# Optimization experiments

Hardware: AMD Instinct MI355X
Metric: run time of the kernel (lower is better)

Reference implementation:

```python
import jax, jax.numpy as jnp
import numpy as np

N = 50000
E = 800000
IN_CH = 128
HID = 64
HEADS = 4
OUT_CH = 64
NEG_SLOPE = 0.2


def add_self_loops(edge_index, num_nodes):
    loops = jnp.arange(num_nodes, dtype=edge_index.dtype)
    src = jnp.concatenate([edge_index[0], loops])
    dst = jnp.concatenate([edge_index[1], loops])
    return src, dst


def gat_layer(x, src, dst, W, a_src, a_dst, b, heads, out_ch, concat):
    n = x.shape[0]
    h = (x @ W).reshape(n, heads, out_ch)              # [N,H,C]
    al_src = jnp.einsum('nhc,hc->nh', h, a_src)        # [N,H]
    al_dst = jnp.einsum('nhc,hc->nh', h, a_dst)        # [N,H]
    e = jax.nn.leaky_relu(al_src[src] + al_dst[dst], NEG_SLOPE)  # [Et,H]
    # segment softmax over incoming edges of each destination node
    m = jax.ops.segment_max(e, dst, num_segments=n)
    ex = jnp.exp(e - m[dst])
    denom = jax.ops.segment_sum(ex, dst, num_segments=n)
    alpha = ex / (denom[dst] + 1e-16)                  # [Et,H]
    msg = h[src] * alpha[:, :, None]                   # [Et,H,C]
    out = jax.ops.segment_sum(msg, dst, num_segments=n)  # [N,H,C]
    if concat:
        out = out.reshape(n, heads * out_ch)
    else:
        out = out.mean(axis=1)
    return out + b


def setup_inputs() -> dict:
    key = jax.random.key(0)
    ks = jax.random.split(key, 10)
    x = jax.random.normal(ks[0], (N, IN_CH), dtype=jnp.float32)
    edge_index = jax.random.randint(ks[1], (2, E), 0, N, dtype=jnp.int64)
    s1 = 1.0 / np.sqrt(IN_CH)
    W1 = jax.random.normal(ks[2], (IN_CH, HEADS * HID), dtype=jnp.float32) * s1
    a_src1 = jax.random.normal(ks[3], (HEADS, HID), dtype=jnp.float32) * 0.1
    a_dst1 = jax.random.normal(ks[4], (HEADS, HID), dtype=jnp.float32) * 0.1
    b1 = jnp.zeros((HEADS * HID,), dtype=jnp.float32)
    s2 = 1.0 / np.sqrt(HEADS * HID)
    W2 = jax.random.normal(ks[5], (HEADS * HID, OUT_CH), dtype=jnp.float32) * s2
    a_src2 = jax.random.normal(ks[6], (1, OUT_CH), dtype=jnp.float32) * 0.1
    a_dst2 = jax.random.normal(ks[7], (1, OUT_CH), dtype=jnp.float32) * 0.1
    b2 = jnp.zeros((OUT_CH,), dtype=jnp.float32)
    return {"x": x, "edge_index": edge_index, "W1": W1, "a_src1": a_src1,
            "a_dst1": a_dst1, "b1": b1, "W2": W2, "a_src2": a_src2,
            "a_dst2": a_dst2, "b2": b2}


def reference(x, edge_index, W1, a_src1, a_dst1, b1, W2, a_src2, a_dst2, b2):
    src, dst = add_self_loops(edge_index, x.shape[0])
    h = gat_layer(x, src, dst, W1, a_src1, a_dst1, b1, HEADS, HID, True)
    h = jax.nn.elu(h)
    h = gat_layer(h, src, dst, W2, a_src2, a_dst2, b2, 1, OUT_CH, False)
    return jax.nn.elu(h)
```

## Files before the change

kernel.cpp:

```cpp
#include <hip/hip_runtime.h>
#include <hip/hip_bf16.h>
#include <cstdint>
#include <cstddef>


#define CAP 96

typedef float f32x4 __attribute__((ext_vector_type(4)));
typedef __fp16 f16x8 __attribute__((ext_vector_type(8)));

static __device__ __forceinline__ float lrelu02(float x) { return x > 0.f ? x : 0.2f * x; }
static __device__ __forceinline__ float eluf(float x)    { return x > 0.f ? x : __expf(x) - 1.f; }

__global__ __launch_bounds__(256) void kD_kernel(const float* __restrict__ A,
                                                 const float* __restrict__ W1,
                                                 __fp16* __restrict__ C,
                                                 const float* __restrict__ a_src,
                                                 const float* __restrict__ a_dst,
                                                 float* __restrict__ als,
                                                 float* __restrict__ ald,
                                                 const int* __restrict__ ei,
                                                 int* __restrict__ cnt,
                                                 int* __restrict__ sidx,
                                                 const float* __restrict__ W2,
                                                 __fp16* __restrict__ w2t,
                                                 int M, int e, int gb, int cb) {
    __shared__ __fp16 sm[17920];
    int b = blockIdx.x;
    int t = threadIdx.x;
    if (b >= gb) {
        if (b < gb + cb) {
            int* sflag = (int*)sm;
            if (t < 64) {
                int m = e < 64 ? e : 64;
                int z = (t < m && ei[2 * t + 1] == 0) ? 1 : 0;
                unsigned long long bal = __ballot(z);
                if (t == 0) *sflag = (__popcll(bal) >= m / 2 + 1) ? 1 : 0;
            }
            __syncthreads();
            int f = *sflag;
            int i = (b - gb) * 256 + t;
            if (i < e) {
                int s = f ? ei[2 * i] : ei[i];
                int d = f ? ei[2 * (e + i)] : ei[e + i];
                int pos = atomicAdd(&cnt[d], 1);
                if (pos < CAP) sidx[d * CAP + pos] = s;
            }
        } else {
            int j = (b - gb - cb) * 256 + t;
            if (j < 16384) {
                int nn = j >> 8, k = j & 255;
                w2t[j] = (__fp16)W2[k * 64 + nn];
            }
        }
        return;
    }
    #define AS(r, c)  sm[(r) * 40 + (c)]
    #define BST(r, c) sm[2560 + (r) * 40 + (c)]
    #define CS(r, c)  sm[(r) * 264 + (c)]
    float* sa = (float*)(sm + 16896);
    float* sd = (float*)(sm + 17408);
    int wv = t >> 6, l = t & 63;
    int lm = l & 15, kq = l >> 4;
    int bm = b * 64;
    sa[t] = a_src[t];
    sd[t] = a_dst[t];
    f32x4 zero = {0.f, 0.f, 0.f, 0.f};
    f32x4 acc[4][4] = {{zero, zero, zero, zero}, {zero, zero, zero, zero},
                       {zero, zero, zero, zero}, {zero, zero, zero, zero}};
    int arow = t >> 2, achunk = (t & 3) * 8;
    for (int k0 = 0; k0 < 128; k0 += 32) {
        {
            int gr = bm + arow;
            f16x8 av;
            if (gr < M) {
                const float* ap = A + (size_t)gr * 128 + k0 + achunk;
                float4 a0 = *(const float4*)(ap + 0);
                float4 a1 = *(const float4*)(ap + 4);
                av[0] = (__fp16)a0.x; av[1] = (__fp16)a0.y; av[2] = (__fp16)a0.z; av[3] = (__fp16)a0.w;
                av[4] = (__fp16)a1.x; av[5] = (__fp16)a1.y; av[6] = (__fp16)a1.z; av[7] = (__fp16)a1.w;
            } else { f16x8 z = {0,0,0,0,0,0,0,0}; av = z; }
            *(f16x8*)&AS(arow, achunk) = av;
        }
        {
            #pragma unroll
            for (int bc = 0; bc < 4; ++bc) {
                f16x8 bh;
                #pragma unroll
                for (int j = 0; j < 8; ++j)
                    bh[j] = (__fp16)W1[(size_t)(k0 + bc * 8 + j) * 256 + t];
                *(f16x8*)&BST(t, bc * 8) = bh;
            }
        }
        __syncthreads();
        #pragma unroll
        for (int nt = 0; nt < 4; ++nt) {
            f16x8 bfrag = *(const f16x8*)&BST(wv * 64 + nt * 16 + lm, kq * 8);
            #pragma unroll
            for (int mt = 0; mt < 4; ++mt) {
                f16x8 afrag = *(const f16x8*)&AS(mt * 16 + lm, kq * 8);
                acc[mt][nt] = __builtin_amdgcn_mfma_f32_16x16x32_f16(afrag, bfrag, acc[mt][nt], 0, 0, 0);
            }
        }
        __syncthreads();
    }
    #pragma unroll
    for (int mt = 0; mt < 4; ++mt)
        #pragma unroll
        for (int nt = 0; nt < 4; ++nt)
            #pragma unroll
            for (int r = 0; r < 4; ++r)
                CS(mt * 16 + kq * 4 + r, wv * 64 + nt * 16 + lm) = (__fp16)acc[mt][nt][r];
    __syncthreads();
    {
        int row = t >> 2, head = t & 3;
        int gr = bm + row;
        f16x8 c[8];
        #pragma unroll
        for (int q = 0; q < 8; ++q) c[q] = *(const f16x8*)&CS(row, head * 64 + q * 8);
        float ps = 0.f, pd = 0.f;
        #pragma unroll
        for (int q = 0; q < 8; ++q)
            #pragma unroll
            for (int j = 0; j < 8; ++j) {
                float v = (float)c[q][j];
                ps += v * sa[head * 64 + q * 8 + j];
                pd += v * sd[head * 64 + q * 8 + j];
            }
        if (gr < M) {
            f16x8* gp = (f16x8*)(C + (size_t)gr * 256 + head * 64);
            #pragma unroll
            for (int q = 0; q < 8; ++q) gp[q] = c[q];
            als[gr * 4 + head] = ps;
            ald[gr * 4 + head] = pd;
        }
    }
    #undef AS
    #undef BST
    #undef CS
}

__global__ __launch_bounds__(256) void agg1_kernel(const __fp16* __restrict__ h1,
                                                   const int* __restrict__ sidx,
                                                   const int* __restrict__ cnt,
                                                   const float* __restrict__ als,
                                                   const float* __restrict__ ald,
                                                   const float* __restrict__ b1,
                                                   __fp16* __restrict__ x2, int n) {
    int t = threadIdx.x, wv = t >> 6, l = t & 63;
    int node = blockIdx.x * 4 + wv;
    if (node >= n) return;
    int le = l & 31, halfE = l >> 5;
    int head = le >> 3;
    float aldn = ald[node * 4 + head];
    int cn = cnt[node];
    cn = cn < CAP ? cn : CAP;
    int p0 = node * CAP;
    float acc[8] = {0.f, 0.f, 0.f, 0.f, 0.f, 0.f, 0.f, 0.f};
    float accw = 0.f;
    auto bodyS = [&](int s) {
        float wt = __expf(lrelu02(als[s * 4 + head] + aldn));
        accw += wt;
        f16x8 r = *(const f16x8*)(h1 + (size_t)s * 256 + le * 8);
        #pragma unroll
        for (int j = 0; j < 8; ++j) acc[j] += wt * (float)r[j];
    };
    auto body = [&](int p) { bodyS(sidx[p]); };
    int p = p0 + halfE, pend = p0 + cn;
    for (; p + 6 < pend; p += 8) { body(p); body(p + 2); body(p + 4); body(p + 6); }
    for (; p < pend; p += 2) body(p);
    if (halfE == 0) bodyS(node);
    #pragma unroll
    for (int j = 0; j < 8; ++j) acc[j] += __shfl_down(acc[j], 32);
    accw += __shfl_down(accw, 32);
    if (l < 32) {
        float rd = 1.f / (accw + 1e-16f);
        f16x8 o;
        #pragma unroll
        for (int j = 0; j < 8; ++j) {
            float v = acc[j] * rd + b1[le * 8 + j];
            o[j] = (__fp16)eluf(v);
        }
        *(f16x8*)(x2 + (size_t)node * 256 + le * 8) = o;
    }
}

__global__ __launch_bounds__(256) void gemm2_kernel(const __fp16* __restrict__ A,
                                                    const __fp16* __restrict__ w2t,
                                                    __fp16* __restrict__ C,
                                                    const float* __restrict__ a_src,
                                                    const float* __restrict__ a_dst,
                                                    float* __restrict__ als,
                                                    float* __restrict__ ald, int M) {
    __shared__ __fp16 sm[9216];
    #define AS(r, c)  sm[(r) * 72 + (c)]
    #define BST(r, c) sm[4608 + (r) * 72 + (c)]
    #define CS(r, c)  sm[(r) * 72 + (c)]
    int t = threadIdx.x;
    int wv = t >> 6, l = t & 63;
    int lm = l & 15, kq = l >> 4;
    int bm = blockIdx.x * 64;
    f32x4 zero = {0.f, 0.f, 0.f, 0.f};
    f32x4 acc[4] = {zero, zero, zero, zero};
    int arow = t >> 2, akp = (t & 3) * 16;
    int bn = t & 63, bkc = (t >> 6) * 16;
    for (int k0 = 0; k0 < 256; k0 += 64) {
        {
            int gr = bm + arow;
            f16x8 av0, av1;
            if (gr < M) {
                const __fp16* ap = A + (size_t)gr * 256 + k0 + akp;
                av0 = *(const f16x8*)(ap);
                av1 = *(const f16x8*)(ap + 8);
            } else { f16x8 z = {0,0,0,0,0,0,0,0}; av0 = z; av1 = z; }
            *(f16x8*)&AS(arow, akp) = av0;
            *(f16x8*)&AS(arow, akp + 8) = av1;
        }
        {
            const __fp16* bp = w2t + (size_t)bn * 256 + k0 + bkc;
            *(f16x8*)&BST(bn, bkc) = *(const f16x8*)(bp);
            *(f16x8*)&BST(bn, bkc + 8) = *(const f16x8*)(bp + 8);
        }
        __syncthreads();
        #pragma unroll
        for (int ki = 0; ki < 2; ++ki) {
            int kc = ki * 32 + kq * 8;
            f16x8 bfrag = *(const f16x8*)&BST(wv * 16 + lm, kc);
            #pragma unroll
            for (int mt = 0; mt < 4; ++mt) {
                f16x8 afrag = *(const f16x8*)&AS(mt * 16 + lm, kc);
                acc[mt] = __builtin_amdgcn_mfma_f32_16x16x32_f16(afrag, bfrag, acc[mt], 0, 0, 0);
            }
        }
        __syncthreads();
    }
    #pragma unroll
    for (int mt = 0; mt < 4; ++mt)
        #pragma unroll
        for (int r = 0; r < 4; ++r)
            CS(mt * 16 + kq * 4 + r, wv * 16 + lm) = (__fp16)acc[mt][r];
    __syncthreads();
    {
        int row = t >> 2, ch = (t & 3) * 16;
        int gr = bm + row;
        f16x8 c0 = *(const f16x8*)&CS(row, ch);
        f16x8 c1 = *(const f16x8*)&CS(row, ch + 8);
        if (gr < M) {
            f16x8* gp = (f16x8*)(C + (size_t)gr * 64 + ch);
            gp[0] = c0; gp[1] = c1;
        }
        float ps = 0.f, pd = 0.f;
        #pragma unroll
        for (int j = 0; j < 8; ++j) {
            float v0 = (float)c0[j], v1 = (float)c1[j];
            ps += v0 * a_src[ch + j] + v1 * a_src[ch + 8 + j];
            pd += v0 * a_dst[ch + j] + v1 * a_dst[ch + 8 + j];
        }
        ps += __shfl_down(ps, 2); ps += __shfl_down(ps, 1);
        pd += __shfl_down(pd, 2); pd += __shfl_down(pd, 1);
        if ((t & 3) == 0 && gr < M) {
            als[gr] = ps;
            ald[gr] = pd;
        }
    }
    #undef AS
    #undef BST
    #undef CS
}

__global__ __launch_bounds__(256) void agg2_kernel(const __fp16* __restrict__ h2,
                                                   const int* __restrict__ sidx,
                                                   const int* __restrict__ cnt,
                                                   const float* __restrict__ als,
                                                   const float* __restrict__ ald,
                                                   const float* __restrict__ b2,
                                                   float* __restrict__ out, int n) {
    int t = threadIdx.x, wv = t >> 6, l = t & 63;
    int node = blockIdx.x * 4 + wv;
    if (node >= n) return;
    int slot = l >> 3, cq = l & 7;
    float aldn = ald[node];
    int cn = cnt[node];
    cn = cn < CAP ? cn : CAP;
    int p0 = node * CAP;
    float acc[8] = {0.f, 0.f, 0.f, 0.f, 0.f, 0.f, 0.f, 0.f};
    float accw = 0.f;
    auto bodyS = [&](int s) {
        float wt = __expf(lrelu02(als[s] + aldn));
        accw += wt;
        f16x8 r = *(const f16x8*)(h2 + (size_t)s * 64 + cq * 8);
        #pragma unroll
        for (int j = 0; j < 8; ++j) acc[j] += wt * (float)r[j];
    };
    auto body = [&](int p) { bodyS(sidx[p]); };
    int p = p0 + slot, pend = p0 + cn;
    for (; p + 24 < pend; p += 32) { body(p); body(p + 8); body(p + 16); body(p + 24); }
    for (; p < pend; p += 8) body(p);
    if (slot == 0) bodyS(node);
    #pragma unroll
    for (int j = 0; j < 8; ++j) {
        acc[j] += __shfl_down(acc[j], 32);
        acc[j] += __shfl_down(acc[j], 16);
        acc[j] += __shfl_down(acc[j], 8);
    }
    accw += __shfl_down(accw, 32);
    accw += __shfl_down(accw, 16);
    accw += __shfl_down(accw, 8);
    if (l < 8) {
        float rd = 1.f / (accw + 1e-16f);
        float4 o0, o1;
        o0.x = eluf(acc[0] * rd + b2[cq * 8 + 0]);
        o0.y = eluf(acc[1] * rd + b2[cq * 8 + 1]);
        o0.z = eluf(acc[2] * rd + b2[cq * 8 + 2]);
        o0.w = eluf(acc[3] * rd + b2[cq * 8 + 3]);
        o1.x = eluf(acc[4] * rd + b2[cq * 8 + 4]);
        o1.y = eluf(acc[5] * rd + b2[cq * 8 + 5]);
        o1.z = eluf(acc[6] * rd + b2[cq * 8 + 6]);
        o1.w = eluf(acc[7] * rd + b2[cq * 8 + 7]);
        float4* gp = (float4*)(out + (size_t)node * 64 + cq * 8);
        gp[0] = o0; gp[1] = o1;
    }
}

extern "C" void kernel_launch(void* const* d_in, const int* in_sizes, int n_in,
                              void* d_out, int out_size, void* d_ws, size_t ws_size,
                              hipStream_t stream) {
    const float* x   = (const float*)d_in[0];
    const int*   ei  = (const int*)d_in[1];
    const float* W1  = (const float*)d_in[2];
    const float* as1 = (const float*)d_in[3];
    const float* ad1 = (const float*)d_in[4];
    const float* b1  = (const float*)d_in[5];
    const float* W2  = (const float*)d_in[6];
    const float* as2 = (const float*)d_in[7];
    const float* ad2 = (const float*)d_in[8];
    const float* b2  = (const float*)d_in[9];
    float* out = (float*)d_out;

    const int n  = in_sizes[0] / 128;
    const int e  = in_sizes[1] / 2;

    char* w = (char*)d_ws;
    size_t off = 0;
    auto take = [&](size_t bytes) -> void* {
        void* p = w + off;
        off = (off + bytes + 255) & ~(size_t)255;
        return p;
    };
    __fp16* h1h = (__fp16*)take((size_t)n * 256 * 2);
    __fp16* x2h = (__fp16*)take((size_t)n * 256 * 2);
    __fp16* h2h = (__fp16*)take((size_t)n * 64 * 2);
    __fp16* w2t = (__fp16*)take((size_t)64 * 256 * 2);
    float* al1s = (float*)take((size_t)n * 4 * 4);
    float* al1d = (float*)take((size_t)n * 4 * 4);
    float* al2s = (float*)take((size_t)n * 4);
    float* al2d = (float*)take((size_t)n * 4);
    int* cnt    = (int*)take((size_t)n * 4);
    int* sidx   = (int*)take((size_t)n * CAP * 4);

    const int gb = (n + 63) / 64;
    const int cb = (e + 255) / 256;
    const int pb = (16384 + 255) / 256;

    hipMemsetAsync(cnt, 0, (size_t)n * 4, stream);
    kD_kernel<<<gb + cb + pb, 256, 0, stream>>>(x, W1, h1h, as1, ad1, al1s, al1d,
                                                ei, cnt, sidx, W2, w2t, n, e, gb, cb);
    agg1_kernel<<<(n + 3) / 4, 256, 0, stream>>>(h1h, sidx, cnt, al1s, al1d, b1, x2h, n);
    gemm2_kernel<<<(n + 63) / 64, 256, 0, stream>>>(x2h, w2t, h2h, as2, ad2, al2s, al2d, n);
    agg2_kernel<<<(n + 3) / 4, 256, 0, stream>>>(h2h, sidx, cnt, al2s, al2d, b2, out, n);
}
```

Measured before the change: 265.1 us.

## Pre-transpose W1 to fp16 in a prep kernel and widen GEMM K-step

A new prep kernel converts and transposes W1 and W2 to fp16 and zeroes the edge counters, replacing the memset and the in-GEMM strided fp32 W1 loads with contiguous fp16 vector loads. The fused kernel now puts edge-bucketing blocks first, and the GEMM loop uses a K-step of 64 with A fragments hoisted and larger LDS tiles. This cuts redundant per-block W1 conversion and halves the barrier count, at the cost of an extra kernel launch and more shared memory per block.

```diff
diff --git a/kernel.cpp b/kernel.cpp
--- a/kernel.cpp
+++ b/kernel.cpp
@@ -12,8 +12,26 @@
 static __device__ __forceinline__ float lrelu02(float x) { return x > 0.f ? x : 0.2f * x; }
 static __device__ __forceinline__ float eluf(float x)    { return x > 0.f ? x : __expf(x) - 1.f; }
 
+__global__ __launch_bounds__(256) void k0_kernel(const float* __restrict__ W1,
+                                                 const float* __restrict__ W2,
+                                                 __fp16* __restrict__ w1t,
+                                                 __fp16* __restrict__ w2t,
+                                                 int* __restrict__ cnt, int n) {
+    int i = blockIdx.x * 256 + threadIdx.x;
+    if (i < 32768) {
+        int nn = i & 255, k = i >> 8;
+        w1t[nn * 128 + k] = (__fp16)W1[k * 256 + nn];
+    } else if (i < 49152) {
+        int j = i - 32768;
+        int nn = j & 63, k = j >> 6;
+        w2t[nn * 256 + k] = (__fp16)W2[k * 64 + nn];
+    } else if (i - 49152 < n) {
+        cnt[i - 49152] = 0;
+    }
+}
+
 __global__ __launch_bounds__(256) void kD_kernel(const float* __restrict__ A,
-                                                 const float* __restrict__ W1,
+                                                 const __fp16* __restrict__ w1t,
                                                  __fp16* __restrict__ C,
                                                  const float* __restrict__ a_src,
                                                  const float* __restrict__ a_dst,
@@ -22,84 +40,82 @@
                                                  const int* __restrict__ ei,
                                                  int* __restrict__ cnt,
                                                  int* __restrict__ sidx,
-                                                 const float* __restrict__ W2,
-                                                 __fp16* __restrict__ w2t,
-                                                 int M, int e, int gb, int cb) {
-    __shared__ __fp16 sm[17920];
+                                                 int M, int e, int cb) {
+    __shared__ __fp16 sm[24064];
     int b = blockIdx.x;
     int t = threadIdx.x;
-    if (b >= gb) {
-        if (b < gb + cb) {
-            int* sflag = (int*)sm;
-            if (t < 64) {
-                int m = e < 64 ? e : 64;
-                int z = (t < m && ei[2 * t + 1] == 0) ? 1 : 0;
-                unsigned long long bal = __ballot(z);
-                if (t == 0) *sflag = (__popcll(bal) >= m / 2 + 1) ? 1 : 0;
-            }
-            __syncthreads();
-            int f = *sflag;
-            int i = (b - gb) * 256 + t;
-            if (i < e) {
-                int s = f ? ei[2 * i] : ei[i];
-                int d = f ? ei[2 * (e + i)] : ei[e + i];
-                int pos = atomicAdd(&cnt[d], 1);
-                if (pos < CAP) sidx[d * CAP + pos] = s;
-            }
-        } else {
-            int j = (b - gb - cb) * 256 + t;
-            if (j < 16384) {
-                int nn = j >> 8, k = j & 255;
-                w2t[j] = (__fp16)W2[k * 64 + nn];
-            }
+    if (b < cb) {
+        int* sflag = (int*)sm;
+        if (t < 64) {
+            int m = e < 64 ? e : 64;
+            int z = (t < m && ei[2 * t + 1] == 0) ? 1 : 0;
+            unsigned long long bal = __ballot(z);
+            if (t == 0) *sflag = (__popcll(bal) >= m / 2 + 1) ? 1 : 0;
+        }
+        __syncthreads();
+        int f = *sflag;
+        int i = b * 256 + t;
+        if (i < e) {
+            int s = f ? ei[2 * i] : ei[i];
+            int d = f ? ei[2 * (e + i)] : ei[e + i];
+            int pos = atomicAdd(&cnt[d], 1);
+            if (pos < CAP) sidx[d * CAP + pos] = s;
         }
         return;
     }
-    #define AS(r, c)  sm[(r) * 40 + (c)]
-    #define BST(r, c) sm[2560 + (r) * 40 + (c)]
+    #define AS(r, c)  sm[(r) * 72 + (c)]
+    #define BST(r, c) sm[4608 + (r) * 72 + (c)]
     #define CS(r, c)  sm[(r) * 264 + (c)]
-    float* sa = (float*)(sm + 16896);
-    float* sd = (float*)(sm + 17408);
+    float* sa = (float*)(sm + 23040);
+    float* sd = (float*)(sm + 23552);
     int wv = t >> 6, l = t & 63;
     int lm = l & 15, kq = l >> 4;
-    int bm = b * 64;
+    int bm = (b - cb) * 64;
     sa[t] = a_src[t];
     sd[t] = a_dst[t];
     f32x4 zero = {0.f, 0.f, 0.f, 0.f};
     f32x4 acc[4][4] = {{zero, zero, zero, zero}, {zero, zero, zero, zero},
                        {zero, zero, zero, zero}, {zero, zero, zero, zero}};
-    int arow = t >> 2, achunk = (t & 3) * 8;
-    for (int k0 = 0; k0 < 128; k0 += 32) {
+    int arow = t >> 2, akp = (t & 3) * 16;
+    for (int k0 = 0; k0 < 128; k0 += 64) {
         {
             int gr = bm + arow;
-            f16x8 av;
+            f16x8 av0, av1;
             if (gr < M) {
-                const float* ap = A + (size_t)gr * 128 + k0 + achunk;
+                const float* ap = A + (size_t)gr * 128 + k0 + akp;
                 float4 a0 = *(const float4*)(ap + 0);
                 float4 a1 = *(const float4*)(ap + 4);
-                av[0] = (__fp16)a0.x; av[1] = (__fp16)a0.y; av[2] = (__fp16)a0.z; av[3] = (__fp16)a0.w;
-                av[4] = (__fp16)a1.x; av[5] = (__fp16)a1.y; av[6] = (__fp16)a1.z; av[7] = (__fp16)a1.w;
-            } else { f16x8 z = {0,0,0,0,0,0,0,0}; av = z; }
-            *(f16x8*)&AS(arow, achunk) = av;
+                float4 a2 = *(const float4*)(ap + 8);
+                float4 a3 = *(const float4*)(ap + 12);
+                av0[0] = (__fp16)a0.x; av0[1] = (__fp16)a0.y; av0[2] = (__fp16)a0.z; av0[3] = (__fp16)a0.w;
+                av0[4] = (__fp16)a1.x; av0[5] = (__fp16)a1.y; av0[6] = (__fp16)a1.z; av0[7] = (__fp16)a1.w;
+                av1[0] = (__fp16)a2.x; av1[1] = (__fp16)a2.y; av1[2] = (__fp16)a2.z; av1[3] = (__fp16)a2.w;
+                av1[4] = (__fp16)a3.x; av1[5] = (__fp16)a3.y; av1[6] = (__fp16)a3.z; av1[7] = (__fp16)a3.w;
+            } else {
+                f16x8 z = {0,0,0,0,0,0,0,0}; av0 = z; av1 = z;
+            }
+            *(f16x8*)&AS(arow, akp) = av0;
+            *(f16x8*)&AS(arow, akp + 8) = av1;
         }
         {
-            #pragma unroll
-            for (int bc = 0; bc < 4; ++bc) {
-                f16x8 bh;
+            const __fp16* bp = w1t + (size_t)t * 128 + k0;
+            #pragma unroll
+            for (int c = 0; c < 8; ++c)
+                *(f16x8*)&BST(t, c * 8) = *(const f16x8*)(bp + c * 8);
+        }
+        __syncthreads();
+        #pragma unroll
+        for (int ki = 0; ki < 2; ++ki) {
+            int kc = ki * 32 + kq * 8;
+            f16x8 af[4];
+            #pragma unroll
+            for (int mt = 0; mt < 4; ++mt) af[mt] = *(const f16x8*)&AS(mt * 16 + lm, kc);
+            #pragma unroll
+            for (int nt = 0; nt < 4; ++nt) {
+                f16x8 bfrag = *(const f16x8*)&BST(wv * 64 + nt * 16 + lm, kc);
                 #pragma unroll
-                for (int j = 0; j < 8; ++j)
-                    bh[j] = (__fp16)W1[(size_t)(k0 + bc * 8 + j) * 256 + t];
-                *(f16x8*)&BST(t, bc * 8) = bh;
-            }
-        }
-        __syncthreads();
-        #pragma unroll
-        for (int nt = 0; nt < 4; ++nt) {
-            f16x8 bfrag = *(const f16x8*)&BST(wv * 64 + nt * 16 + lm, kq * 8);
-            #pragma unroll
-            for (int mt = 0; mt < 4; ++mt) {
-                f16x8 afrag = *(const f16x8*)&AS(mt * 16 + lm, kq * 8);
-                acc[mt][nt] = __builtin_amdgcn_mfma_f32_16x16x32_f16(afrag, bfrag, acc[mt][nt], 0, 0, 0);
+                for (int mt = 0; mt < 4; ++mt)
+                    acc[mt][nt] = __builtin_amdgcn_mfma_f32_16x16x32_f16(af[mt], bfrag, acc[mt][nt], 0, 0, 0);
             }
         }
         __syncthreads();
@@ -350,6 +366,7 @@
     __fp16* h1h = (__fp16*)take((size_t)n * 256 * 2);
     __fp16* x2h = (__fp16*)take((size_t)n * 256 * 2);
     __fp16* h2h = (__fp16*)take((size_t)n * 64 * 2);
+    __fp16* w1t = (__fp16*)take((size_t)256 * 128 * 2);
     __fp16* w2t = (__fp16*)take((size_t)64 * 256 * 2);
     float* al1s = (float*)take((size_t)n * 4 * 4);
     float* al1d = (float*)take((size_t)n * 4 * 4);
@@ -358,13 +375,12 @@
     int* cnt    = (int*)take((size_t)n * 4);
     int* sidx   = (int*)take((size_t)n * CAP * 4);
 
+    const int cb = (e + 255) / 256;
     const int gb = (n + 63) / 64;
-    const int cb = (e + 255) / 256;
-    const int pb = (16384 + 255) / 256;
-
-    hipMemsetAsync(cnt, 0, (size_t)n * 4, stream);
-    kD_kernel<<<gb + cb + pb, 256, 0, stream>>>(x, W1, h1h, as1, ad1, al1s, al1d,
-                                                ei, cnt, sidx, W2, w2t, n, e, gb, cb);
+
+    k0_kernel<<<(49152 + n + 255) / 256, 256, 0, stream>>>(W1, W2, w1t, w2t, cnt, n);
+    kD_kernel<<<cb + gb, 256, 0, stream>>>(x, w1t, h1h, as1, ad1, al1s, al1d,
+                                           ei, cnt, sidx, n, e, cb);
     agg1_kernel<<<(n + 3) / 4, 256, 0, stream>>>(h1h, sidx, cnt, al1s, al1d, b1, x2h, n);
     gemm2_kernel<<<(n + 63) / 64, 256, 0, stream>>>(x2h, w2t, h2h, as2, ad2, al2s, al2d, n);
     agg2_kernel<<<(n + 3) / 4, 256, 0, stream>>>(h2h, sidx, cnt, al2s, al2d, b2, out, n);
```

After: 269.8 us. About the same (+1.8%).
